# Kernel optimization log

Hardware: AMD Instinct MI355X
Metric: run time of the kernel (lower is better)

Reference implementation:

```python
import jax, jax.numpy as jnp
import numpy as np

B, N, XS = 32, 200000, 256
SCALE = 100.0      # generator.scale_factor (grid-units per normalized coord)
CENTER = XS / 2.0  # xmipp_origin
W0_FIRST = 30.0    # SIREN first-layer frequency
SIGMA = 1.0        # gaussianFilterImage sigma
RAD = 3            # gaussian kernel radius (size 7)


def setup_inputs() -> dict:
    key = jax.random.key(0)
    ks = jax.random.split(key, 8)
    rows = jax.random.normal(ks[0], (B, 3), jnp.float32)            # euler angles (rad)
    shifts = jax.random.normal(ks[1], (B, 2), jnp.float32)          # in-plane shifts (px)
    coords = jax.random.uniform(ks[2], (N, 3), jnp.float32, -1.0, 1.0)  # point cloud in [-1,1]^3
    fan_in = 3 * N
    # SIRENFirstLayerInitializer(scale=6.0): U(-scale/fan_in, scale/fan_in)
    W1 = jax.random.uniform(ks[3], (fan_in, 8), jnp.float32, -6.0 / fan_in, 6.0 / fan_in)
    b1 = jnp.zeros((8,), jnp.float32)
    lim = float(np.sqrt(6.0 / 8.0))
    Wh = jax.random.uniform(ks[4], (3, 8, 8), jnp.float32, -lim, lim)
    bh = jnp.zeros((3, 8), jnp.float32)
    W5 = jax.random.normal(ks[5], (8, N), jnp.float32) * 0.05
    b5 = jnp.zeros((N,), jnp.float32)
    ctf = jax.random.uniform(ks[6], (B, XS, XS // 2 + 1), jnp.float32)  # rfft2 CTF filter
    return dict(rows=rows, shifts=shifts, coords=coords, W1=W1, b1=b1,
                Wh=Wh, bh=bh, W5=W5, b5=b5, ctf=ctf)


def euler_zyz(angles):
    # ZYZ Euler rotation matrices, (B,3,3)
    a, b, g = angles[:, 0], angles[:, 1], angles[:, 2]
    def rz(t):
        c, s = jnp.cos(t), jnp.sin(t)
        z, o = jnp.zeros_like(t), jnp.ones_like(t)
        return jnp.stack([jnp.stack([c, -s, z], -1),
                          jnp.stack([s, c, z], -1),
                          jnp.stack([z, z, o], -1)], -2)
    def ry(t):
        c, s = jnp.cos(t), jnp.sin(t)
        z, o = jnp.zeros_like(t), jnp.ones_like(t)
        return jnp.stack([jnp.stack([c, z, s], -1),
                          jnp.stack([z, o, z], -1),
                          jnp.stack([-s, z, c], -1)], -2)
    return rz(a) @ ry(b) @ rz(g)


def reference(rows, shifts, coords, W1, b1, Wh, bh, W5, b5, ctf):
    # --- getRotatedGrid: rotate fixed point cloud by per-image Euler angles ---
    R = euler_zyz(rows)                                   # (B,3,3)
    crot = jnp.einsum('bij,nj->bni', R, coords)           # (B,N,3)
    # --- SIREN MLP on flattened grid (Concatenate+Flatten -> Dense(8) stack) ---
    h = jnp.sin(W0_FIRST * (crot.reshape(B, 3 * N) @ W1 + b1))  # (B,8)
    for i in range(3):
        h = jnp.sin(h @ Wh[i] + bh[i])
    delta = h @ W5 + b5                                   # (B,N) per-point intensities
    # --- scatterImgByPass: bilinear scatter of intensities into (B,XS,XS) ---
    pos = crot[:, :, :2] * SCALE + CENTER - shifts[:, None, :]   # (B,N,2) -> (x,y) px
    x, y = pos[..., 0], pos[..., 1]
    x0 = jnp.floor(x); y0 = jnp.floor(y)
    fx = x - x0; fy = y - y0
    x0i = x0.astype(jnp.int32); y0i = y0.astype(jnp.int32)
    img = jnp.zeros((B, XS, XS), jnp.float32)
    bidx = jnp.arange(B, dtype=jnp.int32)[:, None]
    corners = ((0, 0, (1 - fx) * (1 - fy)), (1, 0, fx * (1 - fy)),
               (0, 1, (1 - fx) * fy), (1, 1, fx * fy))
    for dx, dy, w in corners:
        xi = x0i + dx; yi = y0i + dy
        valid = (xi >= 0) & (xi < XS) & (yi >= 0) & (yi < XS)
        xi = jnp.clip(xi, 0, XS - 1); yi = jnp.clip(yi, 0, XS - 1)
        img = img.at[bidx, yi, xi].add(jnp.where(valid, w * delta, 0.0))
    # --- gaussianFilterImage: separable gaussian blur, sigma=1 ---
    k = jnp.exp(-0.5 * (jnp.arange(-RAD, RAD + 1, dtype=jnp.float32) / SIGMA) ** 2)
    k = k / k.sum()
    dn = ('NCHW', 'OIHW', 'NCHW')
    x4 = img[:, None]                                     # (B,1,XS,XS)
    x4 = jax.lax.conv_general_dilated(x4, k.reshape(1, 1, 2 * RAD + 1, 1),
                                      (1, 1), 'SAME', dimension_numbers=dn)
    x4 = jax.lax.conv_general_dilated(x4, k.reshape(1, 1, 1, 2 * RAD + 1),
                                      (1, 1), 'SAME', dimension_numbers=dn)
    img = x4[:, 0]
    # --- ctfFilterImage: multiply by CTF in Fourier space ---
    F = jnp.fft.rfft2(img)
    out = jnp.fft.irfft2(F * ctf, s=(XS, XS))
    return out.astype(jnp.float32)
```

## Files before the change

kernel.cpp:

```cpp
#include <hip/hip_runtime.h>
#include <math.h>

constexpr int B_  = 32;
constexpr int N_  = 200000;
constexpr int XSZ = 256;
constexpr int PADS = 257;

constexpr int NQ = 4;
constexpr int BQ = 8;
constexpr int NSLAB = 64;
constexpr int BINS_Q = BQ * NSLAB;
constexpr int FILLB = 256;
constexpr int PPB = 782;
constexpr unsigned ENT_N = 1600000;

constexpr float FP_SCALE = 4194304.f;
constexpr float FP_INV   = 1.f / 4194304.f;

constexpr size_t OFF_PART  = 0;
constexpr size_t OFF_H     = 73728;
constexpr size_t OFF_R     = 74752;
constexpr size_t OFF_CNT   = 76800;
constexpr size_t OFF_INTRA = OFF_CNT + 1048576;
constexpr size_t OFF_TOT   = OFF_INTRA + 2097152;
constexpr size_t OFF_BB    = OFF_TOT + 8192;
constexpr size_t OFF_APR   = OFF_BB + 8192;
constexpr size_t OFF_IMG   = OFF_APR + 2097152;
constexpr size_t OFF_ENT   = OFF_IMG + 8388608;
constexpr size_t OFF_DELB  = OFF_ENT + (size_t)NQ * ENT_N * 8;
constexpr size_t OFF_TMP   = OFF_ENT;
constexpr size_t OFF_FC    = OFF_ENT;

__device__ __forceinline__ int rev8(int x) { return (int)(__brev((unsigned)x) >> 24); }

__device__ __forceinline__ void projPxPy(float c0, float c1, float c2,
                                         const float* sRb, const float* ssb,
                                         float& px, float& py) {
  px = fmaf(sRb[0], c0, fmaf(sRb[1], c1, fmaf(sRb[2], c2, ssb[0])));
  py = fmaf(sRb[3], c0, fmaf(sRb[4], c1, fmaf(sRb[5], c2, ssb[1])));
}

__global__ __launch_bounds__(256) void k_reduceT(const float* __restrict__ coords,
                                                 const float* __restrict__ W1,
                                                 float* __restrict__ partial) {
  float acc[72];
  #pragma unroll
  for (int t = 0; t < 72; ++t) acc[t] = 0.f;
  int idx = blockIdx.x * 256 + threadIdx.x;
  for (int n = idx; n < N_; n += 256 * 256) {
    float c0 = coords[n * 3 + 0], c1 = coords[n * 3 + 1], c2 = coords[n * 3 + 2];
    const float4* w4 = reinterpret_cast<const float4*>(W1 + (size_t)n * 24);
    #pragma unroll
    for (int i = 0; i < 3; ++i) {
      float4 wa = w4[i * 2 + 0], wb = w4[i * 2 + 1];
      float wv[8] = {wa.x, wa.y, wa.z, wa.w, wb.x, wb.y, wb.z, wb.w};
      #pragma unroll
      for (int k = 0; k < 8; ++k) {
        acc[i * 8 + k]      += c0 * wv[k];
        acc[24 + i * 8 + k] += c1 * wv[k];
        acc[48 + i * 8 + k] += c2 * wv[k];
      }
    }
  }
  #pragma unroll
  for (int t = 0; t < 72; ++t) {
    float v = acc[t];
    for (int off = 32; off > 0; off >>= 1) v += __shfl_down(v, off, 64);
    acc[t] = v;
  }
  __shared__ float sred[4][72];
  int lane = threadIdx.x & 63, wv_ = threadIdx.x >> 6;
  if (lane == 0) {
    #pragma unroll
    for (int t = 0; t < 72; ++t) sred[wv_][t] = acc[t];
  }
  __syncthreads();
  if (threadIdx.x < 72) {
    int t = threadIdx.x;
    partial[blockIdx.x * 72 + t] = sred[0][t] + sred[1][t] + sred[2][t] + sred[3][t];
  }
}

__global__ __launch_bounds__(128) void k_batch(const float* __restrict__ partial,
                                               const float* __restrict__ rows,
                                               const float* __restrict__ b1,
                                               const float* __restrict__ Wh,
                                               const float* __restrict__ bh,
                                               float* __restrict__ hbuf,
                                               float* __restrict__ Rbuf) {
  __shared__ float T[72];
  int tid = threadIdx.x;
  if (tid < 72) {
    double s = 0.0;
    for (int i = 0; i < 256; ++i) s += (double)partial[i * 72 + tid];
    T[tid] = (float)s;
  }
  __syncthreads();
  if (tid < B_) {
    int b = tid;
    float al = rows[b * 3 + 0], be = rows[b * 3 + 1], ga = rows[b * 3 + 2];
    float sa, ca, sb, cb, sg, cg;
    sincosf(al, &sa, &ca); sincosf(be, &sb, &cb); sincosf(ga, &sg, &cg);
    float R[3][3];
    R[0][0] = ca * cb * cg - sa * sg; R[0][1] = -ca * cb * sg - sa * cg; R[0][2] = ca * sb;
    R[1][0] = sa * cb * cg + ca * sg; R[1][1] = -sa * cb * sg + ca * cg; R[1][2] = sa * sb;
    R[2][0] = -sb * cg;               R[2][1] = sb * sg;                 R[2][2] = cb;
    float h[8];
    #pragma unroll
    for (int k = 0; k < 8; ++k) {
      float z = b1[k];
      #pragma unroll
      for (int i = 0; i < 3; ++i)
        #pragma unroll
        for (int j = 0; j < 3; ++j)
          z += R[i][j] * T[(j * 3 + i) * 8 + k];
      h[k] = sinf(30.f * z);
    }
    for (int l = 0; l < 3; ++l) {
      float nh[8];
      #pragma unroll
      for (int k2 = 0; k2 < 8; ++k2) {
        float z = bh[l * 8 + k2];
        #pragma unroll
        for (int k1 = 0; k1 < 8; ++k1) z += h[k1] * Wh[l * 64 + k1 * 8 + k2];
        nh[k2] = sinf(z);
      }
      #pragma unroll
      for (int k = 0; k < 8; ++k) h[k] = nh[k];
    }
    #pragma unroll
    for (int k = 0; k < 8; ++k) hbuf[b * 8 + k] = h[k];
    #pragma unroll
    for (int i = 0; i < 3; ++i)
      #pragma unroll
      for (int j = 0; j < 3; ++j) Rbuf[b * 9 + i * 3 + j] = R[i][j];
  }
}

__global__ __launch_bounds__(512) void k_count(const float* __restrict__ coords,
                                               const float* __restrict__ Rbuf,
                                               const float* __restrict__ shifts,
                                               unsigned short* __restrict__ cnt) {
  __shared__ float sR[BQ][6];
  __shared__ float ss[BQ][2];
  __shared__ unsigned hist[BINS_Q];
  int tid = threadIdx.x;
  int q = blockIdx.x >> 8;
  int fb = blockIdx.x & 255;
  if (tid < BQ) {
    int b = q * BQ + tid;
    sR[tid][0] = Rbuf[b * 9 + 0] * 100.f; sR[tid][1] = Rbuf[b * 9 + 1] * 100.f; sR[tid][2] = Rbuf[b * 9 + 2] * 100.f;
    sR[tid][3] = Rbuf[b * 9 + 3] * 100.f; sR[tid][4] = Rbuf[b * 9 + 4] * 100.f; sR[tid][5] = Rbuf[b * 9 + 5] * 100.f;
    ss[tid][0] = 128.f - shifts[b * 2 + 0];
    ss[tid][1] = 128.f - shifts[b * 2 + 1];
  }
  hist[tid] = 0;
  __syncthreads();
  int pbase = fb * PPB;
  #pragma unroll
  for (int k = 0; k < 2; ++k) {
    int off = tid + (k << 9);
    int n = pbase + off;
    if (off < PPB && n < N_) {
      float c0 = coords[n * 3], c1 = coords[n * 3 + 1], c2 = coords[n * 3 + 2];
      #pragma unroll
      for (int b = 0; b < BQ; ++b) {
        float px, py;
        projPxPy(c0, c1, c2, sR[b], ss[b], px, py);
        if (px >= -1.f && px < 256.f && py >= -1.f && py < 256.f) {
          int y0 = (int)floorf(py);
          int slab = (y0 < 0 ? 0 : y0) >> 2;
          atomicAdd(&hist[b * NSLAB + slab], 1u);
        }
      }
    }
  }
  __syncthreads();
  cnt[(size_t)blockIdx.x * BINS_Q + tid] = (unsigned short)hist[tid];
}

__global__ __launch_bounds__(256) void k_offA(const unsigned short* __restrict__ cnt,
                                              unsigned* __restrict__ intra,
                                              unsigned* __restrict__ totals) {
  int q = blockIdx.x >> 9;
  int bin = blockIdx.x & 511;
  int t = threadIdx.x;
  size_t cbase = ((size_t)q * FILLB + t) * BINS_Q + bin;
  unsigned orig = cnt[cbase];
  unsigned v = orig;
  int lane = t & 63, wid = t >> 6;
  #pragma unroll
  for (int d = 1; d < 64; d <<= 1) { unsigned u = __shfl_up(v, d, 64); if (lane >= d) v += u; }
  __shared__ unsigned wsum[4];
  if (lane == 63) wsum[wid] = v;
  __syncthreads();
  unsigned woff = 0;
  #pragma unroll
  for (int w = 0; w < 4; ++w) if (w < wid) woff += wsum[w];
  intra[cbase] = woff + v - orig;
  if (t == 255) totals[q * BINS_Q + bin] = woff + v;
}

__global__ __launch_bounds__(512) void k_offB(const unsigned* __restrict__ totals,
                                              unsigned* __restrict__ binBase) {
  int q = blockIdx.x;
  int t = threadIdx.x;
  unsigned orig = totals[q * BINS_Q + t];
  unsigned v = orig;
  int lane = t & 63, wid = t >> 6;
  #pragma unroll
  for (int d = 1; d < 64; d <<= 1) { unsigned u = __shfl_up(v, d, 64); if (lane >= d) v += u; }
  __shared__ unsigned wsum[8];
  if (lane == 63) wsum[wid] = v;
  __syncthreads();
  unsigned woff = 0;
  #pragma unroll
  for (int w = 0; w < 8; ++w) if (w < wid) woff += wsum[w];
  binBase[q * BINS_Q + t] = woff + v - orig;
}

__global__ __launch_bounds__(512) void k_fill2(const float* __restrict__ coords,
                                               const float* __restrict__ W5,
                                               const float* __restrict__ b5,
                                               const float* __restrict__ hbuf,
                                               const float* __restrict__ Rbuf,
                                               const float* __restrict__ shifts,
                                               const unsigned* __restrict__ intra,
                                               const unsigned* __restrict__ binBase,
                                               float2* __restrict__ posb,
                                               float* __restrict__ delb) {
  __shared__ float sR[BQ][6];
  __shared__ float ss[BQ][2];
  __shared__ float sh[BQ][8];
  __shared__ unsigned scur[BINS_Q];
  int tid = threadIdx.x;
  int q = blockIdx.x >> 8;
  int fb = blockIdx.x & 255;
  if (tid < BQ) {
    int b = q * BQ + tid;
    sR[tid][0] = Rbuf[b * 9 + 0] * 100.f; sR[tid][1] = Rbuf[b * 9 + 1] * 100.f; sR[tid][2] = Rbuf[b * 9 + 2] * 100.f;
    sR[tid][3] = Rbuf[b * 9 + 3] * 100.f; sR[tid][4] = Rbuf[b * 9 + 4] * 100.f; sR[tid][5] = Rbuf[b * 9 + 5] * 100.f;
    ss[tid][0] = 128.f - shifts[b * 2 + 0];
    ss[tid][1] = 128.f - shifts[b * 2 + 1];
    #pragma unroll
    for (int k = 0; k < 8; ++k) sh[tid][k] = hbuf[b * 8 + k];
  }
  scur[tid] = binBase[q * BINS_Q + tid] + intra[((size_t)q * FILLB + fb) * BINS_Q + tid];
  __syncthreads();
  float2* posq = posb + (size_t)q * ENT_N;
  float*  delq = delb + (size_t)q * ENT_N;
  int pbase = fb * PPB;
  #pragma unroll
  for (int k = 0; k < 2; ++k) {
    int off = tid + (k << 9);
    int n = pbase + off;
    if (off < PPB && n < N_) {
      float c0 = coords[n * 3], c1 = coords[n * 3 + 1], c2 = coords[n * 3 + 2];
      float b5n = b5[n];
      float w5v[8];
      #pragma unroll
      for (int kk = 0; kk < 8; ++kk) w5v[kk] = W5[(size_t)kk * N_ + n];
      #pragma unroll
      for (int b = 0; b < BQ; ++b) {
        float px, py;
        projPxPy(c0, c1, c2, sR[b], ss[b], px, py);
        if (px >= -1.f && px < 256.f && py >= -1.f && py < 256.f) {
          int y0 = (int)floorf(py);
          int slab = (y0 < 0 ? 0 : y0) >> 2;
          int bin = b * NSLAB + slab;
          unsigned slot = atomicAdd(&scur[bin], 1u);
          if (slot < ENT_N) {
            float delta = b5n;
            #pragma unroll
            for (int kk = 0; kk < 8; ++kk) delta = fmaf(sh[b][kk], w5v[kk], delta);
            posq[slot] = make_float2(px, py);
            delq[slot] = delta;
          }
        }
      }
    }
  }
}

__global__ __launch_bounds__(512) void k_scatter2(const float2* __restrict__ posb,
                                                  const float* __restrict__ delb,
                                                  const unsigned* __restrict__ binBase,
                                                  const unsigned* __restrict__ totals,
                                                  float* __restrict__ img,
                                                  float* __restrict__ apron) {
  __shared__ int tile[5 * XSZ];
  int tid = threadIdx.x;
  int q = blockIdx.x >> 9;
  int bin = blockIdx.x & 511;
  int b_local = bin >> 6;
  int s = bin & 63;
  for (int i = tid; i < 5 * XSZ; i += 512) tile[i] = 0;
  __syncthreads();
  unsigned base = binBase[q * BINS_Q + bin];
  unsigned cntv = totals[q * BINS_Q + bin];
  if (base >= ENT_N) cntv = 0;
  else if (base + cntv > ENT_N) cntv = ENT_N - base;
  const float2* posq = posb + (size_t)q * ENT_N;
  const float*  delq = delb + (size_t)q * ENT_N;
  int ybase = s << 2;
  for (unsigned i = tid; i < cntv; i += 512) {
    float2 pp = posq[base + i];
    float delta = delq[base + i];
    float x0f = floorf(pp.x), y0f = floorf(pp.y);
    float fx = pp.x - x0f, fy = pp.y - y0f;
    int x0 = (int)x0f;
    int r0 = (int)y0f - ybase;
    float wy0 = (1.f - fy) * delta * FP_SCALE;
    float wy1 = fy * delta * FP_SCALE;
    bool xl = (x0 >= 0), xr = (x0 <= 254);
    if (r0 >= 0) {
      int c0i = r0 * XSZ + x0;
      if (xl) atomicAdd(&tile[c0i], __float2int_rn((1.f - fx) * wy0));
      if (xr) atomicAdd(&tile[c0i + 1], __float2int_rn(fx * wy0));
    }
    int c1i = (r0 + 1) * XSZ + x0;
    if (xl) atomicAdd(&tile[c1i], __float2int_rn((1.f - fx) * wy1));
    if (xr) atomicAdd(&tile[c1i + 1], __float2int_rn(fx * wy1));
  }
  __syncthreads();
  int b_global = q * BQ + b_local;
  float* imbase = img + (size_t)b_global * 65536 + (size_t)ybase * XSZ;
  for (int i = tid; i < 4 * XSZ; i += 512) imbase[i] = (float)tile[i] * FP_INV;
  if (tid < XSZ) apron[(size_t)(q * BINS_Q + bin) * XSZ + tid] = (float)tile[4 * XSZ + tid] * FP_INV;
}

__global__ __launch_bounds__(256) void k_apron(const float* __restrict__ apron,
                                               float* __restrict__ img) {
  int bid = blockIdx.x;
  int s = bid & 63;
  if (s == 63) return;
  int b = bid >> 6;
  int q = b >> 3, b_local = b & 7;
  int bin = b_local * NSLAB + s;
  int row = (s + 1) << 2;
  float* dst = img + (size_t)b * 65536 + (size_t)row * XSZ;
  dst[threadIdx.x] += apron[(size_t)(q * BINS_Q + bin) * XSZ + threadIdx.x];
}

__device__ __forceinline__ float bwv(int i) {
  const float bw[7] = {0.004433048f, 0.054005582f, 0.242036226f, 0.399050280f,
                       0.242036226f, 0.054005582f, 0.004433048f};
  return bw[i];
}

__global__ __launch_bounds__(256) void k_blurV(const float* __restrict__ in, float* __restrict__ out) {
  int i = blockIdx.x * 256 + threadIdx.x;
  int x = i & 255;
  int y = (i >> 8) & 255;
  const float* p = in + (i & ~65535);
  float s = 0.f;
  #pragma unroll
  for (int d = -3; d <= 3; ++d) {
    int yy = y + d;
    if ((unsigned)yy < XSZ) s += bwv(d + 3) * p[(yy << 8) + x];
  }
  out[i] = s;
}

__global__ __launch_bounds__(256) void k_blurH(const float* __restrict__ in, float* __restrict__ out) {
  int i = blockIdx.x * 256 + threadIdx.x;
  int x = i & 255;
  float s = 0.f;
  #pragma unroll
  for (int d = -3; d <= 3; ++d) {
    int xx = x + d;
    if ((unsigned)xx < XSZ) s += bwv(d + 3) * in[i + d];
  }
  out[i] = s;
}

__device__ __forceinline__ void fft_dif_fwd(float* re, float* im, const float2* tw, int P, int tid) {
  for (int s = 7; s >= 0; --s) {
    __syncthreads();
    int half = 1 << s;
    for (int q = tid; q < (P << 7); q += 256) {
      int p = q >> 7, k = q & 127;
      int j = k & (half - 1);
      int i0 = ((k >> s) << (s + 1)) | j;
      int i1 = i0 + half;
      float* rp = re + p * PADS; float* ip = im + p * PADS;
      float ar = rp[i0], ai = ip[i0], br = rp[i1], bi = ip[i1];
      rp[i0] = ar + br; ip[i0] = ai + bi;
      float tr = ar - br, ti = ai - bi;
      float2 w = tw[j << (7 - s)];
      rp[i1] = tr * w.x - ti * w.y;
      ip[i1] = tr * w.y + ti * w.x;
    }
  }
  __syncthreads();
}

__device__ __forceinline__ void fft_dit_inv(float* re, float* im, const float2* tw, int P, int tid) {
  for (int s = 0; s <= 7; ++s) {
    __syncthreads();
    int half = 1 << s;
    for (int q = tid; q < (P << 7); q += 256) {
      int p = q >> 7, k = q & 127;
      int j = k & (half - 1);
      int i0 = ((k >> s) << (s + 1)) | j;
      int i1 = i0 + half;
      float* rp = re + p * PADS; float* ip = im + p * PADS;
      float2 w = tw[j << (7 - s)];
      float br = rp[i1], bi = ip[i1];
      float tr = br * w.x + bi * w.y;
      float ti = bi * w.x - br * w.y;
      float ar = rp[i0], ai = ip[i0];
      rp[i0] = ar + tr; ip[i0] = ai + ti;
      rp[i1] = ar - tr; ip[i1] = ai - ti;
    }
  }
  __syncthreads();
}

__device__ __forceinline__ void tw_init(float2* tw, int tid) {
  for (int k = tid; k < 128; k += 256) {
    float s_, c_;
    sincosf(-6.2831853071795864769f * (float)k / 256.0f, &s_, &c_);
    tw[k] = make_float2(c_, s_);
  }
}

__global__ __launch_bounds__(256) void k_fft1(const float* __restrict__ img, float2* __restrict__ Fc) {
  __shared__ float re[16 * PADS], im[16 * PADS];
  __shared__ float2 tw[128];
  int tid = threadIdx.x;
  int b = blockIdx.x >> 4;
  int y0 = (blockIdx.x & 15) << 4;
  tw_init(tw, tid);
  const float* src = img + (size_t)b * 65536 + (size_t)y0 * 256;
  for (int q = tid; q < 4096; q += 256) {
    int j = q >> 8, x = q & 255;
    re[j * PADS + x] = src[j * 256 + x];
    im[j * PADS + x] = 0.f;
  }
  fft_dif_fwd(re, im, tw, 16, tid);
  float2* dst = Fc + (size_t)b * 65536;
  for (int q = tid; q < 4096; q += 256) {
    int j = q & 15, i = q >> 4;
    dst[(size_t)i * 256 + y0 + j] = make_float2(re[j * PADS + i], im[j * PADS + i]);
  }
}

__global__ __launch_bounds__(256) void k_fft2(float2* __restrict__ Fc, const float* __restrict__ ctf) {
  __shared__ float re[4 * PADS], im[4 * PADS];
  __shared__ float2 tw[128];
  int tid = threadIdx.x;
  int b = blockIdx.x >> 6;
  int r0 = (blockIdx.x & 63) << 2;
  tw_init(tw, tid);
  float2* base = Fc + (size_t)b * 65536 + (size_t)r0 * 256;
  for (int q = tid; q < 1024; q += 256) {
    int p = q >> 8, y = q & 255;
    float2 v = base[p * 256 + y];
    re[p * PADS + y] = v.x; im[p * PADS + y] = v.y;
  }
  fft_dif_fwd(re, im, tw, 4, tid);
  for (int q = tid; q < 1024; q += 256) {
    int p = q >> 8, iy = q & 255;
    int kx = rev8(r0 + p), ky = rev8(iy);
    float c;
    if (kx <= 128) c = ctf[((size_t)b * 256 + ky) * 129 + kx];
    else           c = ctf[((size_t)b * 256 + ((256 - ky) & 255)) * 129 + (256 - kx)];
    re[p * PADS + iy] *= c; im[p * PADS + iy] *= c;
  }
  fft_dit_inv(re, im, tw, 4, tid);
  for (int q = tid; q < 1024; q += 256) {
    int p = q >> 8, y = q & 255;
    base[p * 256 + y] = make_float2(re[p * PADS + y], im[p * PADS + y]);
  }
}

__global__ __launch_bounds__(256) void k_fft3(const float2* __restrict__ Fc, float* __restrict__ out) {
  __shared__ float re[16 * PADS], im[16 * PADS];
  __shared__ float2 tw[128];
  int tid = threadIdx.x;
  int b = blockIdx.x >> 4;
  int y0 = (blockIdx.x & 15) << 4;
  tw_init(tw, tid);
  const float2* src = Fc + (size_t)b * 65536;
  for (int q = tid; q < 4096; q += 256) {
    int j = q & 15, r = q >> 4;
    float2 v = src[(size_t)r * 256 + y0 + j];
    re[j * PADS + r] = v.x; im[j * PADS + r] = v.y;
  }
  fft_dit_inv(re, im, tw, 16, tid);
  float* dst = out + (size_t)b * 65536 + (size_t)y0 * 256;
  for (int q = tid; q < 4096; q += 256) {
    int j = q >> 8, x = q & 255;
    dst[j * 256 + x] = re[j * PADS + x] * (1.f / 65536.f);
  }
}

extern "C" void kernel_launch(void* const* d_in, const int* in_sizes, int n_in,
                              void* d_out, int out_size, void* d_ws, size_t ws_size,
                              hipStream_t stream) {
  const float* rows   = (const float*)d_in[0];
  const float* shifts = (const float*)d_in[1];
  const float* coords = (const float*)d_in[2];
  const float* W1     = (const float*)d_in[3];
  const float* b1     = (const float*)d_in[4];
  const float* Wh     = (const float*)d_in[5];
  const float* bh     = (const float*)d_in[6];
  const float* W5     = (const float*)d_in[7];
  const float* b5     = (const float*)d_in[8];
  const float* ctf    = (const float*)d_in[9];
  float* out = (float*)d_out;
  char* ws = (char*)d_ws;

  float*          partial = (float*)(ws + OFF_PART);
  float*          hbuf    = (float*)(ws + OFF_H);
  float*          Rbuf    = (float*)(ws + OFF_R);
  unsigned short* cnt     = (unsigned short*)(ws + OFF_CNT);
  unsigned*       intra   = (unsigned*)(ws + OFF_INTRA);
  unsigned*       totals  = (unsigned*)(ws + OFF_TOT);
  unsigned*       binBase = (unsigned*)(ws + OFF_BB);
  float*          apron   = (float*)(ws + OFF_APR);
  float*          img     = (float*)(ws + OFF_IMG);
  float2*         posb    = (float2*)(ws + OFF_ENT);
  float*          delb    = (float*)(ws + OFF_DELB);
  float*          tmp     = (float*)(ws + OFF_TMP);
  float2*         Fc      = (float2*)(ws + OFF_FC);

  k_reduceT<<<256, 256, 0, stream>>>(coords, W1, partial);
  k_batch<<<1, 128, 0, stream>>>(partial, rows, b1, Wh, bh, hbuf, Rbuf);
  k_count<<<NQ * FILLB, 512, 0, stream>>>(coords, Rbuf, shifts, cnt);
  k_offA<<<NQ * BINS_Q, 256, 0, stream>>>(cnt, intra, totals);
  k_offB<<<NQ, 512, 0, stream>>>(totals, binBase);
  k_fill2<<<NQ * FILLB, 512, 0, stream>>>(coords, W5, b5, hbuf, Rbuf, shifts,
                                          intra, binBase, posb, delb);
  k_scatter2<<<NQ * BINS_Q, 512, 0, stream>>>(posb, delb, binBase, totals, img, apron);
  k_apron<<<B_ * NSLAB, 256, 0, stream>>>(apron, img);
  k_blurV<<<B_ * XSZ * XSZ / 256, 256, 0, stream>>>(img, tmp);
  k_blurH<<<B_ * XSZ * XSZ / 256, 256, 0, stream>>>(tmp, img);
  k_fft1<<<B_ * 16, 256, 0, stream>>>(img, Fc);
  k_fft2<<<B_ * 64, 256, 0, stream>>>(Fc, ctf);
  k_fft3<<<B_ * 16, 256, 0, stream>>>(Fc, out);
}
```

Before: 206.6 us.

## Halve slab count and store point index instead of projected position in bins

The binning granularity goes from 64 slabs of 4 rows to 32 slabs of 8 rows per image. This halves the count, prefix-sum and apron buffers and the number of scatter blocks, at the cost of a larger shared-memory tile per block. Bin entries now hold a packed (point index, delta) float2 instead of a separate float2 position plus a float delta. The scatter kernel recomputes the projection from coords and the rotation, trading 4 bytes per entry of write/read traffic for a gathered coords load and a few FMAs.

Measured after the change: 179.6 us. 1.15x faster.

```diff
diff --git a/kernel.cpp b/kernel.cpp
--- a/kernel.cpp
+++ b/kernel.cpp
@@ -8,7 +8,7 @@
 
 constexpr int NQ = 4;
 constexpr int BQ = 8;
-constexpr int NSLAB = 64;
+constexpr int NSLAB = 32;
 constexpr int BINS_Q = BQ * NSLAB;
 constexpr int FILLB = 256;
 constexpr int PPB = 782;
@@ -21,13 +21,12 @@
 constexpr size_t OFF_H     = 73728;
 constexpr size_t OFF_R     = 74752;
 constexpr size_t OFF_CNT   = 76800;
-constexpr size_t OFF_INTRA = OFF_CNT + 1048576;
-constexpr size_t OFF_TOT   = OFF_INTRA + 2097152;
-constexpr size_t OFF_BB    = OFF_TOT + 8192;
-constexpr size_t OFF_APR   = OFF_BB + 8192;
-constexpr size_t OFF_IMG   = OFF_APR + 2097152;
+constexpr size_t OFF_INTRA = OFF_CNT + 524288;
+constexpr size_t OFF_TOT   = OFF_INTRA + 1048576;
+constexpr size_t OFF_BB    = OFF_TOT + 4096;
+constexpr size_t OFF_APR   = OFF_BB + 4096;
+constexpr size_t OFF_IMG   = OFF_APR + 1048576;
 constexpr size_t OFF_ENT   = OFF_IMG + 8388608;
-constexpr size_t OFF_DELB  = OFF_ENT + (size_t)NQ * ENT_N * 8;
 constexpr size_t OFF_TMP   = OFF_ENT;
 constexpr size_t OFF_FC    = OFF_ENT;
 
@@ -154,7 +153,7 @@
     ss[tid][0] = 128.f - shifts[b * 2 + 0];
     ss[tid][1] = 128.f - shifts[b * 2 + 1];
   }
-  hist[tid] = 0;
+  if (tid < BINS_Q) hist[tid] = 0;
   __syncthreads();
   int pbase = fb * PPB;
   #pragma unroll
@@ -169,21 +168,21 @@
         projPxPy(c0, c1, c2, sR[b], ss[b], px, py);
         if (px >= -1.f && px < 256.f && py >= -1.f && py < 256.f) {
           int y0 = (int)floorf(py);
-          int slab = (y0 < 0 ? 0 : y0) >> 2;
+          int slab = (y0 < 0 ? 0 : y0) >> 3;
           atomicAdd(&hist[b * NSLAB + slab], 1u);
         }
       }
     }
   }
   __syncthreads();
-  cnt[(size_t)blockIdx.x * BINS_Q + tid] = (unsigned short)hist[tid];
+  if (tid < BINS_Q) cnt[(size_t)blockIdx.x * BINS_Q + tid] = (unsigned short)hist[tid];
 }
 
 __global__ __launch_bounds__(256) void k_offA(const unsigned short* __restrict__ cnt,
                                               unsigned* __restrict__ intra,
                                               unsigned* __restrict__ totals) {
-  int q = blockIdx.x >> 9;
-  int bin = blockIdx.x & 511;
+  int q = blockIdx.x >> 8;
+  int bin = blockIdx.x & 255;
   int t = threadIdx.x;
   size_t cbase = ((size_t)q * FILLB + t) * BINS_Q + bin;
   unsigned orig = cnt[cbase];
@@ -201,7 +200,7 @@
   if (t == 255) totals[q * BINS_Q + bin] = woff + v;
 }
 
-__global__ __launch_bounds__(512) void k_offB(const unsigned* __restrict__ totals,
+__global__ __launch_bounds__(256) void k_offB(const unsigned* __restrict__ totals,
                                               unsigned* __restrict__ binBase) {
   int q = blockIdx.x;
   int t = threadIdx.x;
@@ -210,12 +209,12 @@
   int lane = t & 63, wid = t >> 6;
   #pragma unroll
   for (int d = 1; d < 64; d <<= 1) { unsigned u = __shfl_up(v, d, 64); if (lane >= d) v += u; }
-  __shared__ unsigned wsum[8];
+  __shared__ unsigned wsum[4];
   if (lane == 63) wsum[wid] = v;
   __syncthreads();
   unsigned woff = 0;
   #pragma unroll
-  for (int w = 0; w < 8; ++w) if (w < wid) woff += wsum[w];
+  for (int w = 0; w < 4; ++w) if (w < wid) woff += wsum[w];
   binBase[q * BINS_Q + t] = woff + v - orig;
 }
 
@@ -227,8 +226,7 @@
                                                const float* __restrict__ shifts,
                                                const unsigned* __restrict__ intra,
                                                const unsigned* __restrict__ binBase,
-                                               float2* __restrict__ posb,
-                                               float* __restrict__ delb) {
+                                               float2* __restrict__ ent) {
   __shared__ float sR[BQ][6];
   __shared__ float ss[BQ][2];
   __shared__ float sh[BQ][8];
@@ -245,10 +243,10 @@
     #pragma unroll
     for (int k = 0; k < 8; ++k) sh[tid][k] = hbuf[b * 8 + k];
   }
-  scur[tid] = binBase[q * BINS_Q + tid] + intra[((size_t)q * FILLB + fb) * BINS_Q + tid];
-  __syncthreads();
-  float2* posq = posb + (size_t)q * ENT_N;
-  float*  delq = delb + (size_t)q * ENT_N;
+  if (tid < BINS_Q)
+    scur[tid] = binBase[q * BINS_Q + tid] + intra[((size_t)q * FILLB + fb) * BINS_Q + tid];
+  __syncthreads();
+  float2* entq = ent + (size_t)q * ENT_N;
   int pbase = fb * PPB;
   #pragma unroll
   for (int k = 0; k < 2; ++k) {
@@ -266,15 +264,14 @@
         projPxPy(c0, c1, c2, sR[b], ss[b], px, py);
         if (px >= -1.f && px < 256.f && py >= -1.f && py < 256.f) {
           int y0 = (int)floorf(py);
-          int slab = (y0 < 0 ? 0 : y0) >> 2;
+          int slab = (y0 < 0 ? 0 : y0) >> 3;
           int bin = b * NSLAB + slab;
           unsigned slot = atomicAdd(&scur[bin], 1u);
           if (slot < ENT_N) {
             float delta = b5n;
             #pragma unroll
             for (int kk = 0; kk < 8; ++kk) delta = fmaf(sh[b][kk], w5v[kk], delta);
-            posq[slot] = make_float2(px, py);
-            delq[slot] = delta;
+            entq[slot] = make_float2(__int_as_float(n), delta);
           }
         }
       }
@@ -282,32 +279,41 @@
   }
 }
 
-__global__ __launch_bounds__(512) void k_scatter2(const float2* __restrict__ posb,
-                                                  const float* __restrict__ delb,
+__global__ __launch_bounds__(512) void k_scatter2(const float2* __restrict__ ent,
+                                                  const float* __restrict__ coords,
+                                                  const float* __restrict__ Rbuf,
+                                                  const float* __restrict__ shifts,
                                                   const unsigned* __restrict__ binBase,
                                                   const unsigned* __restrict__ totals,
                                                   float* __restrict__ img,
                                                   float* __restrict__ apron) {
-  __shared__ int tile[5 * XSZ];
-  int tid = threadIdx.x;
-  int q = blockIdx.x >> 9;
-  int bin = blockIdx.x & 511;
-  int b_local = bin >> 6;
-  int s = bin & 63;
-  for (int i = tid; i < 5 * XSZ; i += 512) tile[i] = 0;
+  __shared__ int tile[9 * XSZ];
+  __shared__ float sA[8];
+  int tid = threadIdx.x;
+  int q = blockIdx.x >> 8;
+  int bin = blockIdx.x & 255;
+  int b_local = bin >> 5;
+  int s = bin & 31;
+  int b_global = q * BQ + b_local;
+  if (tid < 6)      sA[tid] = Rbuf[b_global * 9 + tid] * 100.f;
+  else if (tid < 8) sA[tid] = 128.f - shifts[b_global * 2 + (tid - 6)];
+  for (int i = tid; i < 9 * XSZ; i += 512) tile[i] = 0;
   __syncthreads();
   unsigned base = binBase[q * BINS_Q + bin];
   unsigned cntv = totals[q * BINS_Q + bin];
   if (base >= ENT_N) cntv = 0;
   else if (base + cntv > ENT_N) cntv = ENT_N - base;
-  const float2* posq = posb + (size_t)q * ENT_N;
-  const float*  delq = delb + (size_t)q * ENT_N;
-  int ybase = s << 2;
+  const float2* entq = ent + (size_t)q * ENT_N;
+  int ybase = s << 3;
   for (unsigned i = tid; i < cntv; i += 512) {
-    float2 pp = posq[base + i];
-    float delta = delq[base + i];
-    float x0f = floorf(pp.x), y0f = floorf(pp.y);
-    float fx = pp.x - x0f, fy = pp.y - y0f;
+    float2 e = entq[base + i];
+    int n = __float_as_int(e.x);
+    float delta = e.y;
+    float c0 = coords[n * 3], c1 = coords[n * 3 + 1], c2 = coords[n * 3 + 2];
+    float px, py;
+    projPxPy(c0, c1, c2, sA, sA + 6, px, py);
+    float x0f = floorf(px), y0f = floorf(py);
+    float fx = px - x0f, fy = py - y0f;
     int x0 = (int)x0f;
     int r0 = (int)y0f - ybase;
     float wy0 = (1.f - fy) * delta * FP_SCALE;
@@ -323,21 +329,20 @@
     if (xr) atomicAdd(&tile[c1i + 1], __float2int_rn(fx * wy1));
   }
   __syncthreads();
-  int b_global = q * BQ + b_local;
   float* imbase = img + (size_t)b_global * 65536 + (size_t)ybase * XSZ;
-  for (int i = tid; i < 4 * XSZ; i += 512) imbase[i] = (float)tile[i] * FP_INV;
-  if (tid < XSZ) apron[(size_t)(q * BINS_Q + bin) * XSZ + tid] = (float)tile[4 * XSZ + tid] * FP_INV;
+  for (int i = tid; i < 8 * XSZ; i += 512) imbase[i] = (float)tile[i] * FP_INV;
+  if (tid < XSZ) apron[(size_t)(q * BINS_Q + bin) * XSZ + tid] = (float)tile[8 * XSZ + tid] * FP_INV;
 }
 
 __global__ __launch_bounds__(256) void k_apron(const float* __restrict__ apron,
                                                float* __restrict__ img) {
   int bid = blockIdx.x;
-  int s = bid & 63;
-  if (s == 63) return;
-  int b = bid >> 6;
+  int s = bid & 31;
+  if (s == 31) return;
+  int b = bid >> 5;
   int q = b >> 3, b_local = b & 7;
   int bin = b_local * NSLAB + s;
-  int row = (s + 1) << 2;
+  int row = (s + 1) << 3;
   float* dst = img + (size_t)b * 65536 + (size_t)row * XSZ;
   dst[threadIdx.x] += apron[(size_t)(q * BINS_Q + bin) * XSZ + threadIdx.x];
 }
@@ -521,8 +526,7 @@
   unsigned*       binBase = (unsigned*)(ws + OFF_BB);
   float*          apron   = (float*)(ws + OFF_APR);
   float*          img     = (float*)(ws + OFF_IMG);
-  float2*         posb    = (float2*)(ws + OFF_ENT);
-  float*          delb    = (float*)(ws + OFF_DELB);
+  float2*         ent     = (float2*)(ws + OFF_ENT);
   float*          tmp     = (float*)(ws + OFF_TMP);
   float2*         Fc      = (float2*)(ws + OFF_FC);
 
@@ -530,10 +534,11 @@
   k_batch<<<1, 128, 0, stream>>>(partial, rows, b1, Wh, bh, hbuf, Rbuf);
   k_count<<<NQ * FILLB, 512, 0, stream>>>(coords, Rbuf, shifts, cnt);
   k_offA<<<NQ * BINS_Q, 256, 0, stream>>>(cnt, intra, totals);
-  k_offB<<<NQ, 512, 0, stream>>>(totals, binBase);
+  k_offB<<<NQ, 256, 0, stream>>>(totals, binBase);
   k_fill2<<<NQ * FILLB, 512, 0, stream>>>(coords, W5, b5, hbuf, Rbuf, shifts,
-                                          intra, binBase, posb, delb);
-  k_scatter2<<<NQ * BINS_Q, 512, 0, stream>>>(posb, delb, binBase, totals, img, apron);
+                                          intra, binBase, ent);
+  k_scatter2<<<NQ * BINS_Q, 512, 0, stream>>>(ent, coords, Rbuf, shifts,
+                                              binBase, totals, img, apron);
   k_apron<<<B_ * NSLAB, 256, 0, stream>>>(apron, img);
   k_blurV<<<B_ * XSZ * XSZ / 256, 256, 0, stream>>>(img, tmp);
   k_blurH<<<B_ * XSZ * XSZ / 256, 256, 0, stream>>>(tmp, img);
```
